# Kernel optimization log

Measured on AMD Instinct MI355X. Metric: run time of the kernel, lower is better.

The kernel has to match this reference:

```python
import jax, jax.numpy as jnp
import numpy as np

N_NODES = 131072
N_EDGES = 2097152
N_GRAPHS = 16384
LRELU_ATT = 0.2   # GATConv negative_slope
LRELU_ACT = 0.01  # F.leaky_relu default
BN_EPS = 1e-5


def _gat_layer(x, src, dst, edge_attr, W, a_src, a_dst, We, a_edge, b, H, C, concat, n_nodes):
    # x: [N, Fin]; W: [Fin, H*C]; a_src/a_dst/a_edge: [H, C]; We: [1, H*C]; b: [H*C] or [C]
    h = (x @ W).reshape(-1, H, C)                                   # [N, H, C]
    alpha_src = jnp.einsum('nhc,hc->nh', h, a_src)                  # [N, H]
    alpha_dst = jnp.einsum('nhc,hc->nh', h, a_dst)                  # [N, H]
    he = (edge_attr @ We).reshape(-1, H, C)                          # [E, H, C]
    alpha_e = jnp.einsum('ehc,hc->eh', he, a_edge)                   # [E, H]
    alpha = alpha_src[src] + alpha_dst[dst] + alpha_e                # [E, H]
    alpha = jax.nn.leaky_relu(alpha, LRELU_ATT)
    # edge-softmax over destination nodes (numerically stable)
    amax = jax.ops.segment_max(alpha, dst, num_segments=n_nodes)
    ex = jnp.exp(alpha - amax[dst])
    denom = jax.ops.segment_sum(ex, dst, num_segments=n_nodes)
    att = ex / (denom[dst] + 1e-16)                                  # [E, H]
    out = jax.ops.segment_sum(h[src] * att[:, :, None], dst, num_segments=n_nodes)  # [N, H, C]
    out = out.reshape(n_nodes, H * C) if concat else out.mean(axis=1)
    return out + b


def setup_inputs() -> dict:
    key = jax.random.key(0)
    ks = iter(jax.random.split(key, 64))
    d = {}
    d['x'] = jax.random.normal(next(ks), (N_NODES, 6), dtype=jnp.float32)
    d['edge_index'] = jax.random.randint(next(ks), (2, N_EDGES), 0, N_NODES, dtype=jnp.int32)
    d['edge_weight'] = jax.random.uniform(next(ks), (N_EDGES,), dtype=jnp.float32)
    d['batch'] = jnp.sort(jax.random.randint(next(ks), (N_NODES,), 0, N_GRAPHS, dtype=jnp.int32))
    # GAT layers: (in, out_channels, heads)
    cfgs = [(6, 16, 4), (64, 32, 4), (128, 16, 4), (64, 50, 1)]
    for i, (fin, C, H) in enumerate(cfgs, 1):
        s = 1.0 / np.sqrt(fin)
        d[f'W{i}'] = jax.random.normal(next(ks), (fin, H * C), dtype=jnp.float32) * s
        d[f'as{i}'] = jax.random.normal(next(ks), (H, C), dtype=jnp.float32) * (1.0 / np.sqrt(C))
        d[f'ad{i}'] = jax.random.normal(next(ks), (H, C), dtype=jnp.float32) * (1.0 / np.sqrt(C))
        d[f'We{i}'] = jax.random.normal(next(ks), (1, H * C), dtype=jnp.float32)
        d[f'ae{i}'] = jax.random.normal(next(ks), (H, C), dtype=jnp.float32) * (1.0 / np.sqrt(C))
        out_dim = H * C if i < 4 else C  # concat for 1-3, not layer 4
        d[f'b{i}'] = jnp.zeros((out_dim,), dtype=jnp.float32)
    d['bn_g'] = jnp.ones((50,), dtype=jnp.float32)
    d['bn_b'] = jnp.zeros((50,), dtype=jnp.float32)
    d['bn_rm'] = jax.random.normal(next(ks), (50,), dtype=jnp.float32) * 0.1
    d['bn_rv'] = jnp.abs(jax.random.normal(next(ks), (50,), dtype=jnp.float32)) + 0.5
    for name, (fi, fo) in [('f1', (50, 30)), ('f2', (30, 20)), ('f3', (20, 2))]:
        d[f'W{name}'] = jax.random.normal(next(ks), (fi, fo), dtype=jnp.float32) * (1.0 / np.sqrt(fi))
        d[f'b{name}'] = jnp.zeros((fo,), dtype=jnp.float32)
    return d


def reference(x, edge_index, edge_weight, batch,
              W1, as1, ad1, We1, ae1, b1,
              W2, as2, ad2, We2, ae2, b2,
              W3, as3, ad3, We3, ae3, b3,
              W4, as4, ad4, We4, ae4, b4,
              bn_g, bn_b, bn_rm, bn_rv,
              Wf1, bf1, Wf2, bf2, Wf3, bf3):
    src, dst = edge_index[0], edge_index[1]
    ea = edge_weight[:, None]  # edge_dim = 1
    n = x.shape[0]
    h = jax.nn.leaky_relu(_gat_layer(x, src, dst, ea, W1, as1, ad1, We1, ae1, b1, 4, 16, True, n), LRELU_ACT)
    h = jax.nn.leaky_relu(_gat_layer(h, src, dst, ea, W2, as2, ad2, We2, ae2, b2, 4, 32, True, n), LRELU_ACT)
    h = jax.nn.leaky_relu(_gat_layer(h, src, dst, ea, W3, as3, ad3, We3, ae3, b3, 4, 16, True, n), LRELU_ACT)
    h = _gat_layer(h, src, dst, ea, W4, as4, ad4, We4, ae4, b4, 1, 50, False, n)
    # BatchNorm (eval mode: running stats)
    h = (h - bn_rm) * jax.lax.rsqrt(bn_rv + BN_EPS) * bn_g + bn_b
    h = jax.nn.leaky_relu(h, LRELU_ACT)
    g = jax.ops.segment_sum(h, batch, num_segments=N_GRAPHS)  # global_add_pool
    g = jax.nn.leaky_relu(g @ Wf1 + bf1, LRELU_ACT)  # dropout p=0.2 is a no-op in eval
    g = jax.nn.leaky_relu(g @ Wf2 + bf2, LRELU_ACT)
    return g @ Wf3 + bf3
```

## Files before the change

kernel.cpp:

```cpp
#include <hip/hip_runtime.h>
#include <hip/hip_fp16.h>
#include <math.h>

#define NN 131072
#define NE 2097152
#define NG 16384

__device__ __forceinline__ float lrelu(float x, float s) { return fmaxf(x, s * x); }

template <int H>
__device__ __forceinline__ float sel_h(const float* a, int hsel) {
    if constexpr (H == 1) return a[0];
    else return hsel == 0 ? a[0] : hsel == 1 ? a[1] : hsel == 2 ? a[2] : a[3];
}

__global__ void k_hist(const int* __restrict__ dst, int* __restrict__ cnt, int* __restrict__ rank) {
    int e = blockIdx.x * 256 + threadIdx.x;
    rank[e] = atomicAdd(&cnt[dst[e]], 1);
}

__global__ void k_scan1(const int* __restrict__ cnt, int* __restrict__ rowptr, int* __restrict__ part) {
    __shared__ int s[256];
    int t = threadIdx.x;
    int i = blockIdx.x * 256 + t;
    int v = cnt[i];
    s[t] = v;
    __syncthreads();
    for (int off = 1; off < 256; off <<= 1) {
        int x = (t >= off) ? s[t - off] : 0;
        __syncthreads();
        s[t] += x;
        __syncthreads();
    }
    rowptr[i] = s[t] - v;
    if (t == 255) part[blockIdx.x] = s[255];
}

__global__ void k_scan2(int* part,
                        const float* __restrict__ We1, const float* __restrict__ ae1,
                        const float* __restrict__ We2, const float* __restrict__ ae2,
                        const float* __restrict__ We3, const float* __restrict__ ae3,
                        const float* __restrict__ We4, const float* __restrict__ ae4,
                        float* __restrict__ ceb) {
    __shared__ int s[512];
    int t = threadIdx.x;
    int v = part[t];
    s[t] = v;
    __syncthreads();
    for (int off = 1; off < 512; off <<= 1) {
        int x = (t >= off) ? s[t - off] : 0;
        __syncthreads();
        s[t] += x;
        __syncthreads();
    }
    part[t] = s[t] - v;
    if (t < 4) {
        float c = 0.f;
        for (int i = 0; i < 16; i++) c += We1[t * 16 + i] * ae1[t * 16 + i];
        ceb[t] = c;
    } else if (t < 8) {
        int h = t - 4;
        float c = 0.f;
        for (int i = 0; i < 32; i++) c += We2[h * 32 + i] * ae2[h * 32 + i];
        ceb[t] = c;
    } else if (t < 12) {
        int h = t - 8;
        float c = 0.f;
        for (int i = 0; i < 16; i++) c += We3[h * 16 + i] * ae3[h * 16 + i];
        ceb[t] = c;
    } else if (t == 12) {
        float c = 0.f;
        for (int i = 0; i < 50; i++) c += We4[i] * ae4[i];
        ceb[t] = c;
    }
}

__global__ void k_scan3(int* __restrict__ rowptr, const int* __restrict__ part) {
    int t = threadIdx.x;
    int i = blockIdx.x * 256 + t;
    rowptr[i] = rowptr[i] + part[blockIdx.x];
    if (i == 0) rowptr[NN] = NE;
}

__global__ void k_scatter(const int* __restrict__ src, const int* __restrict__ dst,
                          const float* __restrict__ ew, const int* __restrict__ rowptr,
                          const int* __restrict__ rank, unsigned int* __restrict__ ep) {
    int e = blockIdx.x * 256 + threadIdx.x;
    int d = dst[e];
    int p = rowptr[d] + rank[e];
    unsigned int s = (unsigned int)src[e];
    unsigned int q = (unsigned int)(ew[e] * 32767.f + 0.5f);
    __builtin_nontemporal_store((s << 15) | (q & 0x7fffu), &ep[p]);
}

__device__ __forceinline__ void ep_unpack(unsigned int u, int& s, float& w) {
    s = (int)(u >> 15);
    w = (float)(u & 0x7fffu) * (1.f / 32767.f);
}

template <int FIN, int F, int FR, int H, int C, int ITER>
__global__ __launch_bounds__(256) void k_transform(
    const float* __restrict__ in, const float* __restrict__ W,
    const float* __restrict__ as_, const float* __restrict__ ad_,
    __half* __restrict__ h, float* __restrict__ alpha_s, float* __restrict__ alpha_d) {
    constexpr int TF = F / 16;
    constexpr int XS = 65;
    __shared__ float Wl[FIN * F];
    __shared__ float Xl[FIN * XS];
    int t = threadIdx.x;
    int tfg = t & 15;
    int ng = t >> 4;
    int f0 = tfg * TF;

    for (int i = t; i < FIN * F; i += 256) {
        int ff = i % F;
        Wl[i] = (ff < FR) ? W[(i / F) * FR + ff] : 0.f;
    }
    float asf[TF], adf[TF];
#pragma unroll
    for (int j = 0; j < TF; j++) {
        bool v = (f0 + j) < FR;
        asf[j] = v ? as_[f0 + j] : 0.f;
        adf[j] = v ? ad_[f0 + j] : 0.f;
    }

    for (int it = 0; it < ITER; ++it) {
        int nb = (blockIdx.x * ITER + it) * 64;
        __syncthreads();
        for (int i = t; i < 64 * FIN; i += 256) {
            int nn = i / FIN, kk = i % FIN;
            Xl[kk * XS + nn] = in[(size_t)(nb + nn) * FIN + kk];
        }
        __syncthreads();

        float acc[4][TF];
#pragma unroll
        for (int i = 0; i < 4; i++)
#pragma unroll
            for (int j = 0; j < TF; j++) acc[i][j] = 0.f;

#pragma unroll 2
        for (int k = 0; k < FIN; ++k) {
            float4 xv = *(const float4*)&Xl[k * XS + ng * 4];
            float wv[TF];
#pragma unroll
            for (int j4 = 0; j4 < TF; j4 += 4) {
                float4 w4 = *(const float4*)&Wl[k * F + f0 + j4];
                wv[j4] = w4.x; wv[j4 + 1] = w4.y; wv[j4 + 2] = w4.z; wv[j4 + 3] = w4.w;
            }
            const float xs[4] = {xv.x, xv.y, xv.z, xv.w};
#pragma unroll
            for (int i = 0; i < 4; i++)
#pragma unroll
                for (int j = 0; j < TF; j++) acc[i][j] = fmaf(xs[i], wv[j], acc[i][j]);
        }

#pragma unroll
        for (int i = 0; i < 4; i++) {
            int n = nb + ng * 4 + i;
            __half hv[TF];
            float ps = 0.f, pd = 0.f;
#pragma unroll
            for (int j = 0; j < TF; j++) {
                hv[j] = __float2half(acc[i][j]);
                ps = fmaf(acc[i][j], asf[j], ps);
                pd = fmaf(acc[i][j], adf[j], pd);
            }
            if constexpr (TF == 4) {
                *(uint2*)(h + (size_t)n * F + f0) = *(uint2*)hv;
            } else {
                *(uint4*)(h + (size_t)n * F + f0) = *(uint4*)hv;
            }
            ps += __shfl_xor(ps, 1);
            pd += __shfl_xor(pd, 1);
            ps += __shfl_xor(ps, 2);
            pd += __shfl_xor(pd, 2);
            if constexpr (H == 1) {
                ps += __shfl_xor(ps, 4);
                pd += __shfl_xor(pd, 4);
                ps += __shfl_xor(ps, 8);
                pd += __shfl_xor(pd, 8);
                if (tfg == 0) {
                    alpha_s[n] = ps;
                    alpha_d[n] = pd;
                }
            } else {
                if ((tfg & 3) == 0) {
                    alpha_s[(size_t)n * H + (tfg >> 2)] = ps;
                    alpha_d[(size_t)n * H + (tfg >> 2)] = pd;
                }
            }
        }
    }
}

template <int H, int C, bool FINAL>
__global__ __launch_bounds__(256) void k_aggregate(
    const __half* __restrict__ h, const float* __restrict__ asrc, const float* __restrict__ adst,
    const int* __restrict__ rowptr, const unsigned int* __restrict__ ep,
    const float* __restrict__ ceb, const float* __restrict__ b,
    const float* __restrict__ bn_g, const float* __restrict__ bn_b,
    const float* __restrict__ bn_rm, const float* __restrict__ bn_rv,
    float* __restrict__ out) {
    constexpr int F = H * C;
    constexpr bool P2 = (F > 64);
    constexpr int FSB = P2 ? 256 : 128;
    __shared__ float lds_att[4][64 * H];
    __shared__ int lds_off[4][64];

    int wid = threadIdx.x >> 6;
    int lane = threadIdx.x & 63;
    int half = lane >> 5;
    int hl = lane & 31;
    int n = blockIdx.x * 8 + wid * 2 + half;
    int r0 = rowptr[n];
    int r1 = rowptr[n + 1];
    int deg = r1 - r0;

    float ce[H], ad[H];
#pragma unroll
    for (int hh = 0; hh < H; hh++) ce[hh] = ceb[hh];
    if constexpr (H == 4) {
        float4 adv = ((const float4*)adst)[n];
        ad[0] = adv.x; ad[1] = adv.y; ad[2] = adv.z; ad[3] = adv.w;
    } else {
        ad[0] = adst[n];
    }

    bool val = hl < deg;
    int s_l = 0;
    float w_l = 0.f;
    if (val) ep_unpack(ep[r0 + hl], s_l, w_l);
    float ex_l[H], psum[H];
    if constexpr (H == 4) {
        if (val) {
            float4 v4 = ((const float4*)asrc)[s_l];
            ex_l[0] = __expf(fminf(lrelu(v4.x + ad[0] + w_l * ce[0], 0.2f), 80.f));
            ex_l[1] = __expf(fminf(lrelu(v4.y + ad[1] + w_l * ce[1], 0.2f), 80.f));
            ex_l[2] = __expf(fminf(lrelu(v4.z + ad[2] + w_l * ce[2], 0.2f), 80.f));
            ex_l[3] = __expf(fminf(lrelu(v4.w + ad[3] + w_l * ce[3], 0.2f), 80.f));
        } else {
            ex_l[0] = ex_l[1] = ex_l[2] = ex_l[3] = 0.f;
        }
    } else {
        ex_l[0] = val ? __expf(fminf(lrelu(asrc[s_l] + ad[0] + w_l * ce[0], 0.2f), 80.f)) : 0.f;
    }
#pragma unroll
    for (int hh = 0; hh < H; hh++) psum[hh] = ex_l[hh];
    for (int r = r0 + 32 + hl; r < r1; r += 32) {
        int s;
        float w;
        ep_unpack(ep[r], s, w);
        if constexpr (H == 4) {
            float4 v4 = ((const float4*)asrc)[s];
            psum[0] += __expf(fminf(lrelu(v4.x + ad[0] + w * ce[0], 0.2f), 80.f));
            psum[1] += __expf(fminf(lrelu(v4.y + ad[1] + w * ce[1], 0.2f), 80.f));
            psum[2] += __expf(fminf(lrelu(v4.z + ad[2] + w * ce[2], 0.2f), 80.f));
            psum[3] += __expf(fminf(lrelu(v4.w + ad[3] + w * ce[3], 0.2f), 80.f));
        } else {
            psum[0] += __expf(fminf(lrelu(asrc[s] + ad[0] + w * ce[0], 0.2f), 80.f));
        }
    }
    float rden[H];
#pragma unroll
    for (int hh = 0; hh < H; hh++) {
        float v = psum[hh];
#pragma unroll
        for (int off = 16; off >= 1; off >>= 1) v += __shfl_xor(v, off);
        rden[hh] = 1.f / (v + 1e-16f);
    }

    lds_off[wid][lane] = s_l * FSB;
#pragma unroll
    for (int hh = 0; hh < H; hh++) lds_att[wid][lane * H + hh] = ex_l[hh] * rden[hh];
    __syncthreads();

    int jn = deg < 32 ? deg : 32;
    int base = half * 32;
    const char* hb = (const char*)h;

    if constexpr (P2) {
        int flane = hl & 15;
        int grp = hl >> 4;
        int f0 = 8 * flane;
        int hsel = f0 >> 5;
        float a[8];
#pragma unroll
        for (int i = 0; i < 8; i++) a[i] = 0.f;
#pragma unroll 4
        for (int j = 0; j < jn; j += 2) {
            int je = base + j + grp;
            int off = lds_off[wid][je];
            float att = lds_att[wid][je * H + hsel];
            uint4 p = *(const uint4*)(hb + (size_t)(off + flane * 16));
            const __half2* hp = (const __half2*)&p;
#pragma unroll
            for (int i = 0; i < 4; i++) {
                a[2 * i] = fmaf(__low2float(hp[i]), att, a[2 * i]);
                a[2 * i + 1] = fmaf(__high2float(hp[i]), att, a[2 * i + 1]);
            }
        }
        if (deg > 32) {
            float rdensel = sel_h<H>(rden, hsel);
            for (int r = r0 + 32; r < r1; ++r) {
                unsigned int u = ep[r];
                int s;
                float w;
                ep_unpack(u, s, w);
                float4 v4 = ((const float4*)asrc)[s];
                float aA[4];
                aA[0] = fminf(lrelu(v4.x + ad[0] + w * ce[0], 0.2f), 80.f);
                aA[1] = fminf(lrelu(v4.y + ad[1] + w * ce[1], 0.2f), 80.f);
                aA[2] = fminf(lrelu(v4.z + ad[2] + w * ce[2], 0.2f), 80.f);
                aA[3] = fminf(lrelu(v4.w + ad[3] + w * ce[3], 0.2f), 80.f);
                float att = __expf(sel_h<H>(aA, hsel)) * rdensel;
                att = (grp == 0) ? att : 0.f;
                uint4 p = *(const uint4*)(hb + (size_t)(s * FSB + flane * 16));
                const __half2* hp = (const __half2*)&p;
#pragma unroll
                for (int i = 0; i < 4; i++) {
                    a[2 * i] = fmaf(__low2float(hp[i]), att, a[2 * i]);
                    a[2 * i + 1] = fmaf(__high2float(hp[i]), att, a[2 * i + 1]);
                }
            }
        }
#pragma unroll
        for (int i = 0; i < 8; i++) a[i] += __shfl_xor(a[i], 16);
        if (hl < 16) {
            float4 o0, o1;
            o0.x = lrelu(a[0] + b[f0], 0.01f);
            o0.y = lrelu(a[1] + b[f0 + 1], 0.01f);
            o0.z = lrelu(a[2] + b[f0 + 2], 0.01f);
            o0.w = lrelu(a[3] + b[f0 + 3], 0.01f);
            o1.x = lrelu(a[4] + b[f0 + 4], 0.01f);
            o1.y = lrelu(a[5] + b[f0 + 5], 0.01f);
            o1.z = lrelu(a[6] + b[f0 + 6], 0.01f);
            o1.w = lrelu(a[7] + b[f0 + 7], 0.01f);
            ((float4*)out)[(size_t)n * 32 + 2 * flane] = o0;
            ((float4*)out)[(size_t)n * 32 + 2 * flane + 1] = o1;
        }
    } else {
        int flane = hl & 7;
        int grp = hl >> 3;
        int f0 = 8 * flane;
        int hsel = (H == 1) ? 0 : (f0 >> 4);
        float a[8];
#pragma unroll
        for (int i = 0; i < 8; i++) a[i] = 0.f;
#pragma unroll 4
        for (int j = 0; j < jn; j += 4) {
            int je = base + j + grp;
            int off = lds_off[wid][je];
            float att = lds_att[wid][je * H + hsel];
            uint4 p = *(const uint4*)(hb + (size_t)(off + flane * 16));
            const __half2* hp = (const __half2*)&p;
#pragma unroll
            for (int i = 0; i < 4; i++) {
                a[2 * i] = fmaf(__low2float(hp[i]), att, a[2 * i]);
                a[2 * i + 1] = fmaf(__high2float(hp[i]), att, a[2 * i + 1]);
            }
        }
        if (deg > 32) {
            float rdensel = sel_h<H>(rden, hsel);
            for (int r = r0 + 32; r < r1; ++r) {
                unsigned int u = ep[r];
                int s;
                float w;
                ep_unpack(u, s, w);
                float aA[H];
                if constexpr (H == 4) {
                    float4 v4 = ((const float4*)asrc)[s];
                    aA[0] = fminf(lrelu(v4.x + ad[0] + w * ce[0], 0.2f), 80.f);
                    aA[1] = fminf(lrelu(v4.y + ad[1] + w * ce[1], 0.2f), 80.f);
                    aA[2] = fminf(lrelu(v4.z + ad[2] + w * ce[2], 0.2f), 80.f);
                    aA[3] = fminf(lrelu(v4.w + ad[3] + w * ce[3], 0.2f), 80.f);
                } else {
                    aA[0] = fminf(lrelu(asrc[s] + ad[0] + w * ce[0], 0.2f), 80.f);
                }
                float att = __expf(sel_h<H>(aA, hsel)) * rdensel;
                att = (grp == 0) ? att : 0.f;
                uint4 p = *(const uint4*)(hb + (size_t)(s * FSB + flane * 16));
                const __half2* hp = (const __half2*)&p;
#pragma unroll
                for (int i = 0; i < 4; i++) {
                    a[2 * i] = fmaf(__low2float(hp[i]), att, a[2 * i]);
                    a[2 * i + 1] = fmaf(__high2float(hp[i]), att, a[2 * i + 1]);
                }
            }
        }
#pragma unroll
        for (int i = 0; i < 8; i++) {
            a[i] += __shfl_xor(a[i], 8);
            a[i] += __shfl_xor(a[i], 16);
        }
        if constexpr (FINAL) {
            if (hl < 7) {
                float o[8];
#pragma unroll
                for (int k = 0; k < 8; k++) {
                    int f = f0 + k;
                    if (f < 50) {
                        float v = a[k] + b[f];
                        v = (v - bn_rm[f]) * rsqrtf(bn_rv[f] + 1e-5f) * bn_g[f] + bn_b[f];
                        o[k] = lrelu(v, 0.01f);
                    } else {
                        o[k] = 0.f;
                    }
                }
                if (f0 < 48) {
                    ((float4*)(out + (size_t)n * 64 + f0))[0] = make_float4(o[0], o[1], o[2], o[3]);
                    ((float4*)(out + (size_t)n * 64 + f0))[1] = make_float4(o[4], o[5], o[6], o[7]);
                } else {
                    ((float2*)(out + (size_t)n * 64 + 48))[0] = make_float2(o[0], o[1]);
                }
            }
        } else {
            if (hl < 8) {
                float4 o0, o1;
                o0.x = lrelu(a[0] + b[f0], 0.01f);
                o0.y = lrelu(a[1] + b[f0 + 1], 0.01f);
                o0.z = lrelu(a[2] + b[f0 + 2], 0.01f);
                o0.w = lrelu(a[3] + b[f0 + 3], 0.01f);
                o1.x = lrelu(a[4] + b[f0 + 4], 0.01f);
                o1.y = lrelu(a[5] + b[f0 + 5], 0.01f);
                o1.z = lrelu(a[6] + b[f0 + 6], 0.01f);
                o1.w = lrelu(a[7] + b[f0 + 7], 0.01f);
                ((float4*)out)[(size_t)n * 16 + 2 * flane] = o0;
                ((float4*)out)[(size_t)n * 16 + 2 * flane + 1] = o1;
            }
        }
    }
}

__global__ __launch_bounds__(256) void k_pool(const float* __restrict__ nodeout, const int* __restrict__ batch,
                                              float* __restrict__ gbuf) {
    int wid = threadIdx.x >> 6;
    int lane = threadIdx.x & 63;
    int g = blockIdx.x * 4 + wid;
    int lo = 0, hi = NN;
    while (lo < hi) {
        int mid = (lo + hi) >> 1;
        if (batch[mid] < g) lo = mid + 1; else hi = mid;
    }
    int s0 = lo;
    hi = NN;
    while (lo < hi) {
        int mid = (lo + hi) >> 1;
        if (batch[mid] < g + 1) lo = mid + 1; else hi = mid;
    }
    int s1 = lo;
    if (lane < 50) {
        float acc = 0.f;
        for (int n = s0; n < s1; ++n) acc += nodeout[(size_t)n * 64 + lane];
        gbuf[(size_t)g * 50 + lane] = acc;
    }
}

__global__ __launch_bounds__(64) void k_mlp(const float* __restrict__ gbuf,
                      const float* __restrict__ Wf1, const float* __restrict__ bf1,
                      const float* __restrict__ Wf2, const float* __restrict__ bf2,
                      const float* __restrict__ Wf3, const float* __restrict__ bf3,
                      float* __restrict__ out) {
    __shared__ float W1[1500], W2[600], W3[40], B1[30], B2[20], B3[2];
    __shared__ float G[64 * 50];
    int t = threadIdx.x;
    for (int i = t; i < 1500; i += 64) W1[i] = Wf1[i];
    for (int i = t; i < 600; i += 64) W2[i] = Wf2[i];
    if (t < 40) W3[t] = Wf3[t];
    if (t < 30) B1[t] = bf1[t];
    if (t < 20) B2[t] = bf2[t];
    if (t < 2) B3[t] = bf3[t];
    int g0 = blockIdx.x * 64;
    for (int i = t; i < 64 * 50; i += 64) G[i] = gbuf[(size_t)g0 * 50 + i];
    __syncthreads();
    float gv[50];
#pragma unroll
    for (int i = 0; i < 50; i++) gv[i] = G[t * 50 + i];
    float h1[30];
#pragma unroll
    for (int j = 0; j < 30; j++) {
        float a = B1[j];
#pragma unroll
        for (int i = 0; i < 50; i++) a += gv[i] * W1[i * 30 + j];
        h1[j] = lrelu(a, 0.01f);
    }
    float h2[20];
#pragma unroll
    for (int j = 0; j < 20; j++) {
        float a = B2[j];
#pragma unroll
        for (int i = 0; i < 30; i++) a += h1[i] * W2[i * 20 + j];
        h2[j] = lrelu(a, 0.01f);
    }
    int g = g0 + t;
    float o0 = B3[0], o1 = B3[1];
#pragma unroll
    for (int i = 0; i < 20; i++) {
        o0 += h2[i] * W3[i * 2];
        o1 += h2[i] * W3[i * 2 + 1];
    }
    ((float2*)out)[g] = make_float2(o0, o1);
}

extern "C" void kernel_launch(void* const* d_in, const int* in_sizes, int n_in,
                              void* d_out, int out_size, void* d_ws, size_t ws_size,
                              hipStream_t stream) {
    const float* x = (const float*)d_in[0];
    const int* ei = (const int*)d_in[1];
    const float* ew = (const float*)d_in[2];
    const int* batch = (const int*)d_in[3];
    const float* W1 = (const float*)d_in[4];
    const float* as1 = (const float*)d_in[5];
    const float* ad1 = (const float*)d_in[6];
    const float* We1 = (const float*)d_in[7];
    const float* ae1 = (const float*)d_in[8];
    const float* b1 = (const float*)d_in[9];
    const float* W2 = (const float*)d_in[10];
    const float* as2 = (const float*)d_in[11];
    const float* ad2 = (const float*)d_in[12];
    const float* We2 = (const float*)d_in[13];
    const float* ae2 = (const float*)d_in[14];
    const float* b2 = (const float*)d_in[15];
    const float* W3 = (const float*)d_in[16];
    const float* as3 = (const float*)d_in[17];
    const float* ad3 = (const float*)d_in[18];
    const float* We3 = (const float*)d_in[19];
    const float* ae3 = (const float*)d_in[20];
    const float* b3 = (const float*)d_in[21];
    const float* W4 = (const float*)d_in[22];
    const float* as4 = (const float*)d_in[23];
    const float* ad4 = (const float*)d_in[24];
    const float* We4 = (const float*)d_in[25];
    const float* ae4 = (const float*)d_in[26];
    const float* b4 = (const float*)d_in[27];
    const float* bn_g = (const float*)d_in[28];
    const float* bn_b = (const float*)d_in[29];
    const float* bn_rm = (const float*)d_in[30];
    const float* bn_rv = (const float*)d_in[31];
    const float* Wf1 = (const float*)d_in[32];
    const float* bf1 = (const float*)d_in[33];
    const float* Wf2 = (const float*)d_in[34];
    const float* bf2 = (const float*)d_in[35];
    const float* Wf3 = (const float*)d_in[36];
    const float* bf3 = (const float*)d_in[37];
    float* out = (float*)d_out;

    const int* src = ei;
    const int* dst = ei + NE;

    char* ws = (char*)d_ws;
    float* feat = (float*)ws;         ws += (size_t)NN * 128 * 4;
    __half* hbuf = (__half*)ws;       ws += (size_t)NN * 128 * 2;
    float* as_buf = (float*)ws;       ws += (size_t)NN * 4 * 4;
    float* ad_buf = (float*)ws;       ws += (size_t)NN * 4 * 4;
    int* cnt = (int*)ws;              ws += (size_t)NN * 4;
    int* rowptr = (int*)ws;           ws += (size_t)(NN + 64) * 4;
    unsigned int* ep = (unsigned int*)ws; ws += (size_t)NE * 4;
    int* part = (int*)ws;             ws += 512 * 4;
    float* ce_buf = (float*)ws;       ws += 64 * 4;
    float* gbuf = (float*)ws;         ws += (size_t)NG * 50 * 4;
    int* rank = (int*)hbuf;

    hipMemsetAsync(cnt, 0, (size_t)NN * 4, stream);
    k_hist<<<NE / 256, 256, 0, stream>>>(dst, cnt, rank);
    k_scan1<<<NN / 256, 256, 0, stream>>>(cnt, rowptr, part);
    k_scan2<<<1, 512, 0, stream>>>(part, We1, ae1, We2, ae2, We3, ae3, We4, ae4, ce_buf);
    k_scan3<<<NN / 256, 256, 0, stream>>>(rowptr, part);
    k_scatter<<<NE / 256, 256, 0, stream>>>(src, dst, ew, rowptr, rank, ep);

    k_transform<6, 64, 64, 4, 16, 4><<<NN / 256, 256, 0, stream>>>(x, W1, as1, ad1, hbuf, as_buf, ad_buf);
    k_aggregate<4, 16, false><<<NN / 8, 256, 0, stream>>>(hbuf, as_buf, ad_buf, rowptr, ep, ce_buf,
                                                          b1, nullptr, nullptr, nullptr, nullptr, feat);
    k_transform<64, 128, 128, 4, 32, 4><<<NN / 256, 256, 0, stream>>>(feat, W2, as2, ad2, hbuf, as_buf, ad_buf);
    k_aggregate<4, 32, false><<<NN / 8, 256, 0, stream>>>(hbuf, as_buf, ad_buf, rowptr, ep, ce_buf + 4,
                                                          b2, nullptr, nullptr, nullptr, nullptr, feat);
    k_transform<128, 64, 64, 4, 16, 4><<<NN / 256, 256, 0, stream>>>(feat, W3, as3, ad3, hbuf, as_buf, ad_buf);
    k_aggregate<4, 16, false><<<NN / 8, 256, 0, stream>>>(hbuf, as_buf, ad_buf, rowptr, ep, ce_buf + 8,
                                                          b3, nullptr, nullptr, nullptr, nullptr, feat);
    k_transform<64, 64, 50, 1, 50, 4><<<NN / 256, 256, 0, stream>>>(feat, W4, as4, ad4, hbuf, as_buf, ad_buf);
    k_aggregate<1, 50, true><<<NN / 8, 256, 0, stream>>>(hbuf, as_buf, ad_buf, rowptr, ep, ce_buf + 12,
                                                         b4, bn_g, bn_b, bn_rm, bn_rv, feat);
    k_pool<<<NG / 4, 256, 0, stream>>>(feat, batch, gbuf);
    k_mlp<<<NG / 64, 64, 0, stream>>>(gbuf, Wf1, bf1, Wf2, bf2, Wf3, bf3, out);
}
```

Baseline: 788.2 us.

## Store intermediate layer features in fp16 and fuse pooling with MLP

Aggregation kernels now write inter-layer node features as fp16 instead of fp32, and the transform kernels read fp16 inputs as half2 pairs. This halves the write and read traffic for the feature buffer between layers. Global add-pooling and the MLP head are merged into one kernel, which removes a launch and the gbuf round trip, and the gather loop unroll goes from 4 to 8. The cost is lower precision in the intermediate activations, and the fused pool kernel has fewer blocks, with 16 serial graphs per wavefront.

```diff
diff --git a/kernel.cpp b/kernel.cpp
--- a/kernel.cpp
+++ b/kernel.cpp
@@ -98,9 +98,9 @@
     w = (float)(u & 0x7fffu) * (1.f / 32767.f);
 }
 
-template <int FIN, int F, int FR, int H, int C, int ITER>
+template <typename TIN, int FIN, int F, int FR, int H, int C, int ITER>
 __global__ __launch_bounds__(256) void k_transform(
-    const float* __restrict__ in, const float* __restrict__ W,
+    const TIN* __restrict__ in, const float* __restrict__ W,
     const float* __restrict__ as_, const float* __restrict__ ad_,
     __half* __restrict__ h, float* __restrict__ alpha_s, float* __restrict__ alpha_d) {
     constexpr int TF = F / 16;
@@ -127,9 +127,18 @@
     for (int it = 0; it < ITER; ++it) {
         int nb = (blockIdx.x * ITER + it) * 64;
         __syncthreads();
-        for (int i = t; i < 64 * FIN; i += 256) {
-            int nn = i / FIN, kk = i % FIN;
-            Xl[kk * XS + nn] = in[(size_t)(nb + nn) * FIN + kk];
+        if constexpr (sizeof(TIN) == 2) {
+            for (int p = t; p < 64 * FIN / 2; p += 256) {
+                int nn = (2 * p) / FIN, kk = (2 * p) % FIN;
+                __half2 v = ((const __half2*)in)[(size_t)(nb + nn) * (FIN / 2) + (kk >> 1)];
+                Xl[kk * XS + nn] = __low2float(v);
+                Xl[(kk + 1) * XS + nn] = __high2float(v);
+            }
+        } else {
+            for (int i = t; i < 64 * FIN; i += 256) {
+                int nn = i / FIN, kk = i % FIN;
+                Xl[kk * XS + nn] = (float)in[(size_t)(nb + nn) * FIN + kk];
+            }
         }
         __syncthreads();
 
@@ -201,7 +210,7 @@
     const float* __restrict__ ceb, const float* __restrict__ b,
     const float* __restrict__ bn_g, const float* __restrict__ bn_b,
     const float* __restrict__ bn_rm, const float* __restrict__ bn_rv,
-    float* __restrict__ out) {
+    __half* __restrict__ out) {
     constexpr int F = H * C;
     constexpr bool P2 = (F > 64);
     constexpr int FSB = P2 ? 256 : 128;
@@ -287,7 +296,7 @@
         float a[8];
 #pragma unroll
         for (int i = 0; i < 8; i++) a[i] = 0.f;
-#pragma unroll 4
+#pragma unroll 8
         for (int j = 0; j < jn; j += 2) {
             int je = base + j + grp;
             int off = lds_off[wid][je];
@@ -327,17 +336,10 @@
 #pragma unroll
         for (int i = 0; i < 8; i++) a[i] += __shfl_xor(a[i], 16);
         if (hl < 16) {
-            float4 o0, o1;
-            o0.x = lrelu(a[0] + b[f0], 0.01f);
-            o0.y = lrelu(a[1] + b[f0 + 1], 0.01f);
-            o0.z = lrelu(a[2] + b[f0 + 2], 0.01f);
-            o0.w = lrelu(a[3] + b[f0 + 3], 0.01f);
-            o1.x = lrelu(a[4] + b[f0 + 4], 0.01f);
-            o1.y = lrelu(a[5] + b[f0 + 5], 0.01f);
-            o1.z = lrelu(a[6] + b[f0 + 6], 0.01f);
-            o1.w = lrelu(a[7] + b[f0 + 7], 0.01f);
-            ((float4*)out)[(size_t)n * 32 + 2 * flane] = o0;
-            ((float4*)out)[(size_t)n * 32 + 2 * flane + 1] = o1;
+            __half ho[8];
+#pragma unroll
+            for (int i = 0; i < 8; i++) ho[i] = __float2half(lrelu(a[i] + b[f0 + i], 0.01f));
+            ((uint4*)out)[(size_t)n * 16 + flane] = *(uint4*)ho;
         }
     } else {
         int flane = hl & 7;
@@ -347,7 +349,7 @@
         float a[8];
 #pragma unroll
         for (int i = 0; i < 8; i++) a[i] = 0.f;
-#pragma unroll 4
+#pragma unroll 8
         for (int j = 0; j < jn; j += 4) {
             int je = base + j + grp;
             int off = lds_off[wid][je];
@@ -395,111 +397,98 @@
         }
         if constexpr (FINAL) {
             if (hl < 7) {
-                float o[8];
+                __half ho[8];
 #pragma unroll
                 for (int k = 0; k < 8; k++) {
                     int f = f0 + k;
+                    float o = 0.f;
                     if (f < 50) {
                         float v = a[k] + b[f];
                         v = (v - bn_rm[f]) * rsqrtf(bn_rv[f] + 1e-5f) * bn_g[f] + bn_b[f];
-                        o[k] = lrelu(v, 0.01f);
-                    } else {
-                        o[k] = 0.f;
+                        o = lrelu(v, 0.01f);
                     }
+                    ho[k] = __float2half(o);
                 }
-                if (f0 < 48) {
-                    ((float4*)(out + (size_t)n * 64 + f0))[0] = make_float4(o[0], o[1], o[2], o[3]);
-                    ((float4*)(out + (size_t)n * 64 + f0))[1] = make_float4(o[4], o[5], o[6], o[7]);
-                } else {
-                    ((float2*)(out + (size_t)n * 64 + 48))[0] = make_float2(o[0], o[1]);
-                }
+                ((uint4*)out)[(size_t)n * 8 + hl] = *(uint4*)ho;
             }
         } else {
             if (hl < 8) {
-                float4 o0, o1;
-                o0.x = lrelu(a[0] + b[f0], 0.01f);
-                o0.y = lrelu(a[1] + b[f0 + 1], 0.01f);
-                o0.z = lrelu(a[2] + b[f0 + 2], 0.01f);
-                o0.w = lrelu(a[3] + b[f0 + 3], 0.01f);
-                o1.x = lrelu(a[4] + b[f0 + 4], 0.01f);
-                o1.y = lrelu(a[5] + b[f0 + 5], 0.01f);
-                o1.z = lrelu(a[6] + b[f0 + 6], 0.01f);
-                o1.w = lrelu(a[7] + b[f0 + 7], 0.01f);
-                ((float4*)out)[(size_t)n * 16 + 2 * flane] = o0;
-                ((float4*)out)[(size_t)n * 16 + 2 * flane + 1] = o1;
-            }
-        }
-    }
-}
-
-__global__ __launch_bounds__(256) void k_pool(const float* __restrict__ nodeout, const int* __restrict__ batch,
-                                              float* __restrict__ gbuf) {
-    int wid = threadIdx.x >> 6;
-    int lane = threadIdx.x & 63;
-    int g = blockIdx.x * 4 + wid;
-    int lo = 0, hi = NN;
-    while (lo < hi) {
-        int mid = (lo + hi) >> 1;
-        if (batch[mid] < g) lo = mid + 1; else hi = mid;
-    }
-    int s0 = lo;
-    hi = NN;
-    while (lo < hi) {
-        int mid = (lo + hi) >> 1;
-        if (batch[mid] < g + 1) lo = mid + 1; else hi = mid;
-    }
-    int s1 = lo;
-    if (lane < 50) {
-        float acc = 0.f;
-        for (int n = s0; n < s1; ++n) acc += nodeout[(size_t)n * 64 + lane];
-        gbuf[(size_t)g * 50 + lane] = acc;
-    }
-}
-
-__global__ __launch_bounds__(64) void k_mlp(const float* __restrict__ gbuf,
-                      const float* __restrict__ Wf1, const float* __restrict__ bf1,
-                      const float* __restrict__ Wf2, const float* __restrict__ bf2,
-                      const float* __restrict__ Wf3, const float* __restrict__ bf3,
-                      float* __restrict__ out) {
+                __half ho[8];
+#pragma unroll
+                for (int i = 0; i < 8; i++) ho[i] = __float2half(lrelu(a[i] + b[f0 + i], 0.01f));
+                ((uint4*)out)[(size_t)n * 8 + flane] = *(uint4*)ho;
+            }
+        }
+    }
+}
+
+__global__ __launch_bounds__(256) void k_pool_mlp(
+    const __half* __restrict__ nodeout, const int* __restrict__ batch,
+    const float* __restrict__ Wf1, const float* __restrict__ bf1,
+    const float* __restrict__ Wf2, const float* __restrict__ bf2,
+    const float* __restrict__ Wf3, const float* __restrict__ bf3,
+    float* __restrict__ out) {
     __shared__ float W1[1500], W2[600], W3[40], B1[30], B2[20], B3[2];
-    __shared__ float G[64 * 50];
+    __shared__ float G[64 * 51];
     int t = threadIdx.x;
-    for (int i = t; i < 1500; i += 64) W1[i] = Wf1[i];
-    for (int i = t; i < 600; i += 64) W2[i] = Wf2[i];
+    for (int i = t; i < 1500; i += 256) W1[i] = Wf1[i];
+    for (int i = t; i < 600; i += 256) W2[i] = Wf2[i];
     if (t < 40) W3[t] = Wf3[t];
     if (t < 30) B1[t] = bf1[t];
     if (t < 20) B2[t] = bf2[t];
     if (t < 2) B3[t] = bf3[t];
     int g0 = blockIdx.x * 64;
-    for (int i = t; i < 64 * 50; i += 64) G[i] = gbuf[(size_t)g0 * 50 + i];
+    int wv = t >> 6, lane = t & 63;
+    for (int k = 0; k < 16; ++k) {
+        int lg = wv * 16 + k;
+        int g = g0 + lg;
+        int lo = 0, hi = NN;
+        while (lo < hi) {
+            int mid = (lo + hi) >> 1;
+            if (batch[mid] < g) lo = mid + 1; else hi = mid;
+        }
+        int s0 = lo;
+        hi = NN;
+        while (lo < hi) {
+            int mid = (lo + hi) >> 1;
+            if (batch[mid] < g + 1) lo = mid + 1; else hi = mid;
+        }
+        int s1 = lo;
+        if (lane < 50) {
+            float acc = 0.f;
+            for (int n = s0; n < s1; ++n) acc += __half2float(nodeout[(size_t)n * 64 + lane]);
+            G[lg * 51 + lane] = acc;
+        }
+    }
     __syncthreads();
-    float gv[50];
-#pragma unroll
-    for (int i = 0; i < 50; i++) gv[i] = G[t * 50 + i];
-    float h1[30];
-#pragma unroll
-    for (int j = 0; j < 30; j++) {
-        float a = B1[j];
-#pragma unroll
-        for (int i = 0; i < 50; i++) a += gv[i] * W1[i * 30 + j];
-        h1[j] = lrelu(a, 0.01f);
-    }
-    float h2[20];
-#pragma unroll
-    for (int j = 0; j < 20; j++) {
-        float a = B2[j];
-#pragma unroll
-        for (int i = 0; i < 30; i++) a += h1[i] * W2[i * 20 + j];
-        h2[j] = lrelu(a, 0.01f);
-    }
-    int g = g0 + t;
-    float o0 = B3[0], o1 = B3[1];
-#pragma unroll
-    for (int i = 0; i < 20; i++) {
-        o0 += h2[i] * W3[i * 2];
-        o1 += h2[i] * W3[i * 2 + 1];
-    }
-    ((float2*)out)[g] = make_float2(o0, o1);
+    if (t < 64) {
+        float gv[50];
+#pragma unroll
+        for (int i = 0; i < 50; i++) gv[i] = G[t * 51 + i];
+        float h1[30];
+#pragma unroll
+        for (int j = 0; j < 30; j++) {
+            float a = B1[j];
+#pragma unroll
+            for (int i = 0; i < 50; i++) a += gv[i] * W1[i * 30 + j];
+            h1[j] = lrelu(a, 0.01f);
+        }
+        float h2[20];
+#pragma unroll
+        for (int j = 0; j < 20; j++) {
+            float a = B2[j];
+#pragma unroll
+            for (int i = 0; i < 30; i++) a += h1[i] * W2[i * 20 + j];
+            h2[j] = lrelu(a, 0.01f);
+        }
+        float o0 = B3[0], o1 = B3[1];
+#pragma unroll
+        for (int i = 0; i < 20; i++) {
+            o0 += h2[i] * W3[i * 2];
+            o1 += h2[i] * W3[i * 2 + 1];
+        }
+        ((float2*)out)[g0 + t] = make_float2(o0, o1);
+    }
 }
 
 extern "C" void kernel_launch(void* const* d_in, const int* in_sizes, int n_in,
@@ -549,7 +538,7 @@
     const int* dst = ei + NE;
 
     char* ws = (char*)d_ws;
-    float* feat = (float*)ws;         ws += (size_t)NN * 128 * 4;
+    __half* feat = (__half*)ws;       ws += (size_t)NN * 128 * 2;
     __half* hbuf = (__half*)ws;       ws += (size_t)NN * 128 * 2;
     float* as_buf = (float*)ws;       ws += (size_t)NN * 4 * 4;
     float* ad_buf = (float*)ws;       ws += (size_t)NN * 4 * 4;
@@ -558,7 +547,6 @@
     unsigned int* ep = (unsigned int*)ws; ws += (size_t)NE * 4;
     int* part = (int*)ws;             ws += 512 * 4;
     float* ce_buf = (float*)ws;       ws += 64 * 4;
-    float* gbuf = (float*)ws;         ws += (size_t)NG * 50 * 4;
     int* rank = (int*)hbuf;
 
     hipMemsetAsync(cnt, 0, (size_t)NN * 4, stream);
@@ -568,18 +556,17 @@
     k_scan3<<<NN / 256, 256, 0, stream>>>(rowptr, part);
     k_scatter<<<NE / 256, 256, 0, stream>>>(src, dst, ew, rowptr, rank, ep);
 
-    k_transform<6, 64, 64, 4, 16, 4><<<NN / 256, 256, 0, stream>>>(x, W1, as1, ad1, hbuf, as_buf, ad_buf);
+    k_transform<float, 6, 64, 64, 4, 16, 4><<<NN / 256, 256, 0, stream>>>(x, W1, as1, ad1, hbuf, as_buf, ad_buf);
     k_aggregate<4, 16, false><<<NN / 8, 256, 0, stream>>>(hbuf, as_buf, ad_buf, rowptr, ep, ce_buf,
                                                           b1, nullptr, nullptr, nullptr, nullptr, feat);
-    k_transform<64, 128, 128, 4, 32, 4><<<NN / 256, 256, 0, stream>>>(feat, W2, as2, ad2, hbuf, as_buf, ad_buf);
+    k_transform<__half, 64, 128, 128, 4, 32, 4><<<NN / 256, 256, 0, stream>>>(feat, W2, as2, ad2, hbuf, as_buf, ad_buf);
     k_aggregate<4, 32, false><<<NN / 8, 256, 0, stream>>>(hbuf, as_buf, ad_buf, rowptr, ep, ce_buf + 4,
                                                           b2, nullptr, nullptr, nullptr, nullptr, feat);
-    k_transform<128, 64, 64, 4, 16, 4><<<NN / 256, 256, 0, stream>>>(feat, W3, as3, ad3, hbuf, as_buf, ad_buf);
+    k_transform<__half, 128, 64, 64, 4, 16, 4><<<NN / 256, 256, 0, stream>>>(feat, W3, as3, ad3, hbuf, as_buf, ad_buf);
     k_aggregate<4, 16, false><<<NN / 8, 256, 0, stream>>>(hbuf, as_buf, ad_buf, rowptr, ep, ce_buf + 8,
                                                           b3, nullptr, nullptr, nullptr, nullptr, feat);
-    k_transform<64, 64, 50, 1, 50, 4><<<NN / 256, 256, 0, stream>>>(feat, W4, as4, ad4, hbuf, as_buf, ad_buf);
+    k_transform<__half, 64, 64, 50, 1, 50, 4><<<NN / 256, 256, 0, stream>>>(feat, W4, as4, ad4, hbuf, as_buf, ad_buf);
     k_aggregate<1, 50, true><<<NN / 8, 256, 0, stream>>>(hbuf, as_buf, ad_buf, rowptr, ep, ce_buf + 12,
                                                          b4, bn_g, bn_b, bn_rm, bn_rv, feat);
-    k_pool<<<NG / 4, 256, 0, stream>>>(feat, batch, gbuf);
-    k_mlp<<<NG / 64, 64, 0, stream>>>(gbuf, Wf1, bf1, Wf2, bf2, Wf3, bf3, out);
-}
+    k_pool_mlp<<<NG / 64, 256, 0, stream>>>(feat, batch, Wf1, bf1, Wf2, bf2, Wf3, bf3, out);
+}
```

Measured after the change: 870.8 us. +10.5%, slower.
